# Performance work log

Hardware: AMD Instinct MI355X
Metric: run time of the kernel (lower is better)

Reference implementation:

```python
import jax, jax.numpy as jnp
import numpy as np

T, S, F, A = 256, 256, 1024, 256


def setup_inputs() -> dict:
    key = jax.random.key(0)
    ks = jax.random.split(key, 7)
    scale = 0.02
    return {
        "batch_data": jax.random.normal(ks[0], (T * S, F), dtype=jnp.float32),
        "a_w": jax.random.normal(ks[1], (F, A), dtype=jnp.float32) * scale,
        "a_b": jax.random.normal(ks[2], (A,), dtype=jnp.float32) * scale,
        "b_w": jax.random.normal(ks[3], (F, A), dtype=jnp.float32) * scale,
        "b_b": jax.random.normal(ks[4], (A,), dtype=jnp.float32) * scale,
        "g_w": jax.random.normal(ks[5], (F, F), dtype=jnp.float32) * scale,
        "g_b": jax.random.normal(ks[6], (F,), dtype=jnp.float32) * scale,
        "s": S,
        "t": T,
    }


def reference(batch_data, a_w, a_b, b_w, b_b, g_w, g_b, s, t):
    # Linear projections then reshape to (t, s, dim)
    theta = (batch_data @ a_w + a_b).reshape(t, s, -1)   # (t, s, A)
    phi = (batch_data @ b_w + b_b).reshape(t, s, -1)     # (t, s, A)
    feats = (batch_data @ g_w + g_b).reshape(t, s, -1)   # (t, s, F)
    # Per-t bilinear attention: theta @ phi^T, no softmax
    attn = jnp.einsum("tsa,tra->tsr", theta, phi)        # (t, s, s)
    results = jnp.einsum("tsr,trf->tsf", attn, feats)    # (t, s, F)
    return results / (s + t)
```

## Files before the change

### kernel.cpp

```cpp
#include <hip/hip_runtime.h>
#include <stdint.h>

#define TT 256
#define SS 256
#define FF 1024
#define AA 256

typedef __attribute__((ext_vector_type(8))) short short8;
typedef __attribute__((ext_vector_type(4))) float floatx4;

__device__ __forceinline__ unsigned short f2bf(float f) {
  unsigned int u = __float_as_uint(f);
  u += 0x7FFFu + ((u >> 16) & 1u);
  return (unsigned short)(u >> 16);
}

__device__ __forceinline__ void gl_lds16(const unsigned short* g, unsigned short* l) {
  __builtin_amdgcn_global_load_lds(
      (__attribute__((address_space(1))) void*)(g),
      (__attribute__((address_space(3))) void*)(l), 16, 0, 0);
}

__global__ void k_transpose_cvt(const float* __restrict__ W,
                                unsigned short* __restrict__ WT,
                                int K, int N) {
  __shared__ float tile[32][33];
  const int bk = blockIdx.x * 32, bn = blockIdx.y * 32;
  const int tx = threadIdx.x, ty = threadIdx.y;
  for (int i = ty; i < 32; i += 8)
    tile[i][tx] = W[(size_t)(bk + i) * N + bn + tx];
  __syncthreads();
  for (int i = ty; i < 32; i += 8)
    WT[(size_t)(bn + i) * K + bk + tx] = f2bf(tile[tx][i]);
}

__global__ __launch_bounds__(256) void k_cvt(const float* __restrict__ in,
                                             unsigned short* __restrict__ out,
                                             unsigned int n8) {
  unsigned int i = blockIdx.x * 256u + threadIdx.x;
  const unsigned int stride = gridDim.x * 256u;
  for (; i < n8; i += stride) {
    const size_t base = (size_t)i * 8;
    const floatx4 v0 = *(const floatx4*)(in + base);
    const floatx4 v1 = *(const floatx4*)(in + base + 4);
    ushort4 h0, h1;
    h0.x = f2bf(v0.x); h0.y = f2bf(v0.y); h0.z = f2bf(v0.z); h0.w = f2bf(v0.w);
    h1.x = f2bf(v1.x); h1.y = f2bf(v1.y); h1.z = f2bf(v1.z); h1.w = f2bf(v1.w);
    *(ushort4*)(out + base) = h0;
    *(ushort4*)(out + base + 4) = h1;
  }
}

__device__ __forceinline__ void stage_half(const unsigned short* G,
                                           unsigned short* L, int tid) {
  const int wave = tid >> 6, lane = tid & 63;
#pragma unroll
  for (int c = 0; c < 2; ++c) {
    const int chunk = c * 8 + wave;
    const int r = chunk * 8 + (lane >> 3);
    const int k8 = (lane & 7) ^ (lane >> 3);
    gl_lds16(G + (size_t)r * FF + k8 * 8, L + chunk * 512);
  }
}

__device__ __forceinline__ short8 ldsfrag(const unsigned short* h, int row,
                                          int col) {
  return *(const short8*)&h[row * 64 + (col ^ ((row & 7) << 3))];
}

__global__ __launch_bounds__(512, 2) void k_proj3(
    const unsigned short* __restrict__ batchH,
    const unsigned short* __restrict__ aT,
    const unsigned short* __restrict__ bT,
    const unsigned short* __restrict__ gT,
    const float* __restrict__ a_b, const float* __restrict__ b_b,
    const float* __restrict__ g_b,
    unsigned short* __restrict__ theta,
    unsigned short* __restrict__ phi,
    unsigned short* __restrict__ featsT,
    int mbase) {
  __shared__ unsigned short lds[65536];
  unsigned short* As = lds;
  unsigned short* Bs = lds + 32768;

  const int nwg = gridDim.x;
  const int hb = blockIdx.x;
  const int logical = (hb & 7) * (nwg >> 3) + (hb >> 3);
  const int nt = logical % 6;
  const int mtile = logical / 6;
  const int m0l = mtile * 256;
  const int m0 = mbase + m0l;

  const unsigned short* Wt; const float* bias; int nb0, mode;
  if (nt == 0)      { Wt = aT; bias = a_b; nb0 = 0;              mode = 0; }
  else if (nt == 1) { Wt = bT; bias = b_b; nb0 = 0;              mode = 1; }
  else              { Wt = gT; bias = g_b; nb0 = (nt - 2) * 256; mode = 2; }

  const int tid = threadIdx.x;
  const int wave = tid >> 6, lane = tid & 63;
  const int wm = wave >> 2, wn = wave & 3;
  const int lr = lane & 15, lq = lane >> 4;
  const int brow = (wn & 1) * 64;

  const unsigned short* Ap = batchH + (size_t)m0l * FF;
  const unsigned short* Bp = Wt + (size_t)nb0 * FF;

  floatx4 acc[8][4];
#pragma unroll
  for (int i = 0; i < 8; i++)
#pragma unroll
    for (int j = 0; j < 4; j++) acc[i][j] = (floatx4)0.0f;

  stage_half(Bp,                Bs + 0 * 8192, tid);
  stage_half(Bp + 128 * FF,     Bs + 1 * 8192, tid);
  stage_half(Ap,                As + 0 * 8192, tid);
  stage_half(Ap + 128 * FF,     As + 1 * 8192, tid);
  stage_half(Bp + 64,           Bs + 2 * 8192, tid);
  stage_half(Bp + 128 * FF + 64, Bs + 3 * 8192, tid);

  short8 af[4][2], bf[4][2];
  const int NKT = FF / 64;

#pragma unroll 1
  for (int kt = 0; kt < NKT; ++kt) {
    const unsigned short* Ah = As + ((kt & 1) * 2 + wm) * 8192;
    const unsigned short* Bh = Bs + ((kt & 1) * 2 + (wn >> 1)) * 8192;
    const int nbuf = 1 - (kt & 1);

    if (kt + 1 < NKT)
      stage_half(Ap + (size_t)(kt + 1) * 64, As + (nbuf * 2 + 0) * 8192, tid);
    if (kt + 1 < NKT) asm volatile("s_waitcnt vmcnt(6)" ::: "memory");
    else              asm volatile("s_waitcnt vmcnt(0)" ::: "memory");
    asm volatile("s_barrier" ::: "memory");
#pragma unroll
    for (int i = 0; i < 4; ++i)
#pragma unroll
      for (int ks = 0; ks < 2; ++ks)
        af[i][ks] = ldsfrag(Ah, i * 16 + lr, ks * 32 + lq * 8);
#pragma unroll
    for (int j = 0; j < 2; ++j)
#pragma unroll
      for (int ks = 0; ks < 2; ++ks)
        bf[j][ks] = ldsfrag(Bh, brow + j * 16 + lr, ks * 32 + lq * 8);
    __builtin_amdgcn_s_setprio(1);
#pragma unroll
    for (int i = 0; i < 4; ++i)
#pragma unroll
      for (int j = 0; j < 2; ++j)
#pragma unroll
        for (int ks = 0; ks < 2; ++ks)
          acc[i][j] = __builtin_amdgcn_mfma_f32_16x16x32_bf16(
              af[i][ks], bf[j][ks], acc[i][j], 0, 0, 0);
    __builtin_amdgcn_s_setprio(0);
    asm volatile("s_barrier" ::: "memory");

    if (kt + 1 < NKT)
      stage_half(Ap + 128 * FF + (size_t)(kt + 1) * 64,
                 As + (nbuf * 2 + 1) * 8192, tid);
#pragma unroll
    for (int j = 0; j < 2; ++j)
#pragma unroll
      for (int ks = 0; ks < 2; ++ks)
        bf[2 + j][ks] = ldsfrag(Bh, brow + (2 + j) * 16 + lr, ks * 32 + lq * 8);
    __builtin_amdgcn_s_setprio(1);
#pragma unroll
    for (int i = 0; i < 4; ++i)
#pragma unroll
      for (int j = 0; j < 2; ++j)
#pragma unroll
        for (int ks = 0; ks < 2; ++ks)
          acc[i][2 + j] = __builtin_amdgcn_mfma_f32_16x16x32_bf16(
              af[i][ks], bf[2 + j][ks], acc[i][2 + j], 0, 0, 0);
    __builtin_amdgcn_s_setprio(0);
    asm volatile("s_barrier" ::: "memory");

    if (kt + 2 < NKT)
      stage_half(Bp + (size_t)(kt + 2) * 64, Bs + ((kt & 1) * 2 + 0) * 8192,
                 tid);
#pragma unroll
    for (int i = 0; i < 4; ++i)
#pragma unroll
      for (int ks = 0; ks < 2; ++ks)
        af[i][ks] = ldsfrag(Ah, 64 + i * 16 + lr, ks * 32 + lq * 8);
    __builtin_amdgcn_s_setprio(1);
#pragma unroll
    for (int i = 0; i < 4; ++i)
#pragma unroll
      for (int j = 0; j < 2; ++j)
#pragma unroll
        for (int ks = 0; ks < 2; ++ks)
          acc[4 + i][j] = __builtin_amdgcn_mfma_f32_16x16x32_bf16(
              af[i][ks], bf[j][ks], acc[4 + i][j], 0, 0, 0);
    __builtin_amdgcn_s_setprio(0);
    asm volatile("s_barrier" ::: "memory");

    if (kt + 2 < NKT)
      stage_half(Bp + 128 * FF + (size_t)(kt + 2) * 64,
                 Bs + ((kt & 1) * 2 + 1) * 8192, tid);
    __builtin_amdgcn_s_setprio(1);
#pragma unroll
    for (int i = 0; i < 4; ++i)
#pragma unroll
      for (int j = 0; j < 2; ++j)
#pragma unroll
        for (int ks = 0; ks < 2; ++ks)
          acc[4 + i][2 + j] = __builtin_amdgcn_mfma_f32_16x16x32_bf16(
              af[i][ks], bf[2 + j][ks], acc[4 + i][2 + j], 0, 0, 0);
    __builtin_amdgcn_s_setprio(0);
    asm volatile("s_barrier" ::: "memory");
  }

#pragma unroll
  for (int fi = 0; fi < 8; ++fi) {
    const int srow = wm * 128 + fi * 16 + lq * 4;
#pragma unroll
    for (int j = 0; j < 4; ++j) {
      const int col = wn * 64 + j * 16 + lr;
      const float bv = bias[nb0 + col];
      if (mode == 2) {
        const int t = m0 >> 8;
        ushort4 h;
        h.x = f2bf(acc[fi][j][0] + bv);
        h.y = f2bf(acc[fi][j][1] + bv);
        h.z = f2bf(acc[fi][j][2] + bv);
        h.w = f2bf(acc[fi][j][3] + bv);
        *(ushort4*)&featsT[((size_t)t * FF + nb0 + col) * SS + srow] = h;
      } else {
        unsigned short* outp = (mode == 0) ? theta : phi;
#pragma unroll
        for (int rr = 0; rr < 4; ++rr)
          outp[(size_t)(m0 + srow + rr) * AA + col] = f2bf(acc[fi][j][rr] + bv);
      }
    }
  }
}

template <bool OUTF32>
__global__ __launch_bounds__(256) void k_gemm_bt(
    const unsigned short* __restrict__ A, const unsigned short* __restrict__ B,
    void* __restrict__ C, int N, int K, long sA, long sB, long sC,
    float scale) {
  __shared__ unsigned short As[128 * 32];
  __shared__ unsigned short Bs[128 * 32];

  const unsigned gx = gridDim.x, gy = gridDim.y;
  unsigned h = (blockIdx.z * gy + blockIdx.y) * gx + blockIdx.x;
  const unsigned nwg = gx * gy * gridDim.z;
  unsigned l = (nwg & 7) ? h : (h & 7) * (nwg >> 3) + (h >> 3);
  const unsigned bx = l % gx; l /= gx;
  const unsigned by = l % gy; const unsigned bz = l / gy;

  const unsigned short* Ab = A + (size_t)bz * sA;
  const unsigned short* Bb = B + (size_t)bz * sB;
  const int n0 = bx * 128, m0 = by * 128;
  const int tid = threadIdx.x, lane = tid & 63, wave = tid >> 6;
  const int wm = wave >> 1, wn = wave & 1, lr = lane & 15, lq = lane >> 4;

  floatx4 acc[4][4];
#pragma unroll
  for (int i = 0; i < 4; i++)
#pragma unroll
    for (int j = 0; j < 4; j++) acc[i][j] = (floatx4)0.0f;

  for (int k0 = 0; k0 < K; k0 += 32) {
    __syncthreads();
    int sl = tid;
    gl_lds16(Ab + (size_t)(m0 + (sl >> 2)) * K + k0 + (sl & 3) * 8,
             &As[wave * 512]);
    gl_lds16(Bb + (size_t)(n0 + (sl >> 2)) * K + k0 + (sl & 3) * 8,
             &Bs[wave * 512]);
    sl = tid + 256;
    gl_lds16(Ab + (size_t)(m0 + (sl >> 2)) * K + k0 + (sl & 3) * 8,
             &As[2048 + wave * 512]);
    gl_lds16(Bb + (size_t)(n0 + (sl >> 2)) * K + k0 + (sl & 3) * 8,
             &Bs[2048 + wave * 512]);
    __syncthreads();

    short8 af[4], bfr[4];
#pragma unroll
    for (int i = 0; i < 4; i++)
      af[i] = *(const short8*)&As[(wm * 64 + i * 16 + lr) * 32 + lq * 8];
#pragma unroll
    for (int j = 0; j < 4; j++)
      bfr[j] = *(const short8*)&Bs[(wn * 64 + j * 16 + lr) * 32 + lq * 8];
#pragma unroll
    for (int i = 0; i < 4; i++)
#pragma unroll
      for (int j = 0; j < 4; j++)
        acc[i][j] = __builtin_amdgcn_mfma_f32_16x16x32_bf16(af[i], bfr[j],
                                                            acc[i][j], 0, 0, 0);
  }

#pragma unroll
  for (int i = 0; i < 4; i++) {
    const int row0 = wm * 64 + i * 16 + lq * 4;
#pragma unroll
    for (int j = 0; j < 4; j++) {
      const int col = wn * 64 + j * 16 + lr;
#pragma unroll
      for (int rr = 0; rr < 4; rr++) {
        const float v = acc[i][j][rr] * scale;
        if (OUTF32) {
          float* Cb = (float*)C + (size_t)bz * sC;
          Cb[(size_t)(m0 + row0 + rr) * N + n0 + col] = v;
        } else {
          unsigned short* Cb = (unsigned short*)C + (size_t)bz * sC;
          Cb[(size_t)(m0 + row0 + rr) * N + n0 + col] = f2bf(v);
        }
      }
    }
  }
}

extern "C" void kernel_launch(void* const* d_in, const int* in_sizes, int n_in,
                              void* d_out, int out_size, void* d_ws,
                              size_t ws_size, hipStream_t stream) {
  const float* batch = (const float*)d_in[0];
  const float* a_w   = (const float*)d_in[1];
  const float* a_b   = (const float*)d_in[2];
  const float* b_w   = (const float*)d_in[3];
  const float* b_b   = (const float*)d_in[4];
  const float* g_w   = (const float*)d_in[5];
  const float* g_b   = (const float*)d_in[6];
  float* out = (float*)d_out;

  unsigned short* ws     = (unsigned short*)d_ws;
  unsigned short* aT     = ws;
  unsigned short* bT     = aT + (size_t)AA * FF;
  unsigned short* gT     = bT + (size_t)AA * FF;
  unsigned short* theta  = gT + (size_t)FF * FF;
  unsigned short* phi    = theta + (size_t)TT * SS * AA;
  unsigned short* featsT = phi + (size_t)TT * SS * AA;
  unsigned short* attn   = featsT + (size_t)TT * FF * SS;

  dim3 tb(32, 8);
  k_transpose_cvt<<<dim3(32, 8),  tb, 0, stream>>>(a_w, aT, FF, AA);
  k_transpose_cvt<<<dim3(32, 8),  tb, 0, stream>>>(b_w, bT, FF, AA);
  k_transpose_cvt<<<dim3(32, 32), tb, 0, stream>>>(g_w, gT, FF, FF);

  const size_t base_bytes  = 238026752ull;
  const size_t batch_bytes = (size_t)TT * SS * FF * 2;
  if (ws_size >= base_bytes + batch_bytes) {
    unsigned short* batchH = attn + (size_t)TT * SS * SS;
    k_cvt<<<2048, 256, 0, stream>>>(batch, batchH,
                                    (unsigned int)((size_t)TT * SS * FF / 8));
    k_proj3<<<6 * 256, 512, 0, stream>>>(batchH, aT, bT, gT, a_b, b_b, g_b,
                                         theta, phi, featsT, 0);
  } else {
    unsigned short* batchH = attn;
    const int CHUNK_ROWS = 16384;
    for (int c = 0; c < 4; c++) {
      const float* src = batch + (size_t)c * CHUNK_ROWS * FF;
      k_cvt<<<2048, 256, 0, stream>>>(
          src, batchH, (unsigned int)((size_t)CHUNK_ROWS * FF / 8));
      k_proj3<<<6 * 64, 512, 0, stream>>>(batchH, aT, bT, gT, a_b, b_b, g_b,
                                          theta, phi, featsT, c * CHUNK_ROWS);
    }
  }

  k_gemm_bt<false><<<dim3(2, 2, TT), 256, 0, stream>>>(
      theta, phi, attn, SS, AA, (long)SS * AA, (long)SS * AA, (long)SS * SS,
      1.0f);

  k_gemm_bt<true><<<dim3(8, 2, TT), 256, 0, stream>>>(
      attn, featsT, out, FF, SS, (long)SS * SS, (long)FF * SS, (long)SS * FF,
      1.0f / 512.0f);
}
```

Before: 439.5 us.

## Replace batched 128x128 attention GEMMs with shared pipelined 256x256 tile kernel

Factors the projection kernel's double-buffered 256x256 MFMA k-loop into macros with a configurable leading dimension. The two per-t batched GEMMs (theta·phiᵀ and attn·feats) now use this deeper-pipelined 512-thread 256x256 tile kernel instead of the simple 128x128 kernel that synchronised every 32-wide k-step. The aim is more data reuse and overlap of loads with compute. In exchange the grid is far smaller (256 and 1024 workgroups), and the projection k-loop now holds a separate af1 fragment set, which uses more registers.

```diff
diff --git a/kernel.cpp b/kernel.cpp
--- a/kernel.cpp
+++ b/kernel.cpp
@@ -51,7 +51,7 @@
   }
 }
 
-__device__ __forceinline__ void stage_half(const unsigned short* G,
+__device__ __forceinline__ void stage_half(const unsigned short* G, int ld,
                                            unsigned short* L, int tid) {
   const int wave = tid >> 6, lane = tid & 63;
 #pragma unroll
@@ -59,7 +59,7 @@
     const int chunk = c * 8 + wave;
     const int r = chunk * 8 + (lane >> 3);
     const int k8 = (lane & 7) ^ (lane >> 3);
-    gl_lds16(G + (size_t)r * FF + k8 * 8, L + chunk * 512);
+    gl_lds16(G + (size_t)r * ld + k8 * 8, L + chunk * 512);
   }
 }
 
@@ -67,6 +67,79 @@
                                           int col) {
   return *(const short8*)&h[row * 64 + (col ^ ((row & 7) << 3))];
 }
+
+#define KLOOP_256(Ap, ldA, Bp, ldB, NKT)                                       \
+  for (int kt = 0; kt < (NKT); ++kt) {                                         \
+    const unsigned short* Ah = As + ((kt & 1) * 2 + wm) * 8192;                \
+    const unsigned short* Bh = Bs + ((kt & 1) * 2 + (wn >> 1)) * 8192;         \
+    const int nbuf = 1 - (kt & 1);                                             \
+    if (kt + 1 < (NKT)) {                                                      \
+      stage_half((Ap) + (size_t)(kt + 1) * 64, (ldA),                          \
+                 As + (nbuf * 2 + 0) * 8192, tid);                             \
+      asm volatile("s_waitcnt vmcnt(6)" ::: "memory");                         \
+    } else {                                                                   \
+      asm volatile("s_waitcnt vmcnt(0)" ::: "memory");                         \
+    }                                                                          \
+    asm volatile("s_barrier" ::: "memory");                                    \
+    _Pragma("unroll") for (int i = 0; i < 4; ++i)                              \
+        _Pragma("unroll") for (int ks = 0; ks < 2; ++ks)                       \
+            af[i][ks] = ldsfrag(Ah, i * 16 + lr, ks * 32 + lq * 8);            \
+    _Pragma("unroll") for (int j = 0; j < 4; ++j)                              \
+        _Pragma("unroll") for (int ks = 0; ks < 2; ++ks)                       \
+            bf[j][ks] = ldsfrag(Bh, brow + j * 16 + lr, ks * 32 + lq * 8);     \
+    __builtin_amdgcn_s_setprio(1);                                             \
+    _Pragma("unroll") for (int i = 0; i < 4; ++i)                              \
+        _Pragma("unroll") for (int j = 0; j < 2; ++j)                          \
+            _Pragma("unroll") for (int ks = 0; ks < 2; ++ks)                   \
+                acc[i][j] = __builtin_amdgcn_mfma_f32_16x16x32_bf16(           \
+                    af[i][ks], bf[j][ks], acc[i][j], 0, 0, 0);                 \
+    __builtin_amdgcn_s_setprio(0);                                             \
+    asm volatile("s_barrier" ::: "memory");                                    \
+    if (kt + 1 < (NKT))                                                        \
+      stage_half((Ap) + 128 * (ldA) + (size_t)(kt + 1) * 64, (ldA),            \
+                 As + (nbuf * 2 + 1) * 8192, tid);                             \
+    _Pragma("unroll") for (int i = 0; i < 4; ++i)                              \
+        _Pragma("unroll") for (int ks = 0; ks < 2; ++ks)                       \
+            af1[i][ks] = ldsfrag(Ah, 64 + i * 16 + lr, ks * 32 + lq * 8);      \
+    __builtin_amdgcn_s_setprio(1);                                             \
+    _Pragma("unroll") for (int i = 0; i < 4; ++i)                              \
+        _Pragma("unroll") for (int j = 0; j < 2; ++j)                          \
+            _Pragma("unroll") for (int ks = 0; ks < 2; ++ks)                   \
+                acc[i][2 + j] = __builtin_amdgcn_mfma_f32_16x16x32_bf16(       \
+                    af[i][ks], bf[2 + j][ks], acc[i][2 + j], 0, 0, 0);         \
+    __builtin_amdgcn_s_setprio(0);                                             \
+    asm volatile("s_barrier" ::: "memory");                                    \
+    if (kt + 2 < (NKT))                                                        \
+      stage_half((Bp) + (size_t)(kt + 2) * 64, (ldB),                          \
+                 Bs + ((kt & 1) * 2 + 0) * 8192, tid);                         \
+    __builtin_amdgcn_s_setprio(1);                                             \
+    _Pragma("unroll") for (int i = 0; i < 4; ++i)                              \
+        _Pragma("unroll") for (int j = 0; j < 2; ++j)                          \
+            _Pragma("unroll") for (int ks = 0; ks < 2; ++ks)                   \
+                acc[4 + i][j] = __builtin_amdgcn_mfma_f32_16x16x32_bf16(       \
+                    af1[i][ks], bf[j][ks], acc[4 + i][j], 0, 0, 0);            \
+    __builtin_amdgcn_s_setprio(0);                                             \
+    asm volatile("s_barrier" ::: "memory");                                    \
+    if (kt + 2 < (NKT))                                                        \
+      stage_half((Bp) + 128 * (ldB) + (size_t)(kt + 2) * 64, (ldB),            \
+                 Bs + ((kt & 1) * 2 + 1) * 8192, tid);                         \
+    __builtin_amdgcn_s_setprio(1);                                             \
+    _Pragma("unroll") for (int i = 0; i < 4; ++i)                              \
+        _Pragma("unroll") for (int j = 0; j < 2; ++j)                          \
+            _Pragma("unroll") for (int ks = 0; ks < 2; ++ks)                   \
+                acc[4 + i][2 + j] = __builtin_amdgcn_mfma_f32_16x16x32_bf16(   \
+                    af1[i][ks], bf[2 + j][ks], acc[4 + i][2 + j], 0, 0, 0);    \
+    __builtin_amdgcn_s_setprio(0);                                             \
+    asm volatile("s_barrier" ::: "memory");                                    \
+  }
+
+#define PROLOGUE_256(Ap, ldA, Bp, ldB)                                         \
+  stage_half((Bp), (ldB), Bs + 0 * 8192, tid);                                 \
+  stage_half((Bp) + 128 * (ldB), (ldB), Bs + 1 * 8192, tid);                   \
+  stage_half((Ap), (ldA), As + 0 * 8192, tid);                                 \
+  stage_half((Ap) + 128 * (ldA), (ldA), As + 1 * 8192, tid);                   \
+  stage_half((Bp) + 64, (ldB), Bs + 2 * 8192, tid);                            \
+  stage_half((Bp) + 128 * (ldB) + 64, (ldB), Bs + 3 * 8192, tid);
 
 __global__ __launch_bounds__(512, 2) void k_proj3(
     const unsigned short* __restrict__ batchH,
@@ -111,104 +184,11 @@
 #pragma unroll
     for (int j = 0; j < 4; j++) acc[i][j] = (floatx4)0.0f;
 
-  stage_half(Bp,                Bs + 0 * 8192, tid);
-  stage_half(Bp + 128 * FF,     Bs + 1 * 8192, tid);
-  stage_half(Ap,                As + 0 * 8192, tid);
-  stage_half(Ap + 128 * FF,     As + 1 * 8192, tid);
-  stage_half(Bp + 64,           Bs + 2 * 8192, tid);
-  stage_half(Bp + 128 * FF + 64, Bs + 3 * 8192, tid);
-
-  short8 af[4][2], bf[4][2];
-  const int NKT = FF / 64;
-
+  short8 af[4][2], af1[4][2], bf[4][2];
+
+  PROLOGUE_256(Ap, FF, Bp, FF)
 #pragma unroll 1
-  for (int kt = 0; kt < NKT; ++kt) {
-    const unsigned short* Ah = As + ((kt & 1) * 2 + wm) * 8192;
-    const unsigned short* Bh = Bs + ((kt & 1) * 2 + (wn >> 1)) * 8192;
-    const int nbuf = 1 - (kt & 1);
-
-    if (kt + 1 < NKT)
-      stage_half(Ap + (size_t)(kt + 1) * 64, As + (nbuf * 2 + 0) * 8192, tid);
-    if (kt + 1 < NKT) asm volatile("s_waitcnt vmcnt(6)" ::: "memory");
-    else              asm volatile("s_waitcnt vmcnt(0)" ::: "memory");
-    asm volatile("s_barrier" ::: "memory");
-#pragma unroll
-    for (int i = 0; i < 4; ++i)
-#pragma unroll
-      for (int ks = 0; ks < 2; ++ks)
-        af[i][ks] = ldsfrag(Ah, i * 16 + lr, ks * 32 + lq * 8);
-#pragma unroll
-    for (int j = 0; j < 2; ++j)
-#pragma unroll
-      for (int ks = 0; ks < 2; ++ks)
-        bf[j][ks] = ldsfrag(Bh, brow + j * 16 + lr, ks * 32 + lq * 8);
-    __builtin_amdgcn_s_setprio(1);
-#pragma unroll
-    for (int i = 0; i < 4; ++i)
-#pragma unroll
-      for (int j = 0; j < 2; ++j)
-#pragma unroll
-        for (int ks = 0; ks < 2; ++ks)
-          acc[i][j] = __builtin_amdgcn_mfma_f32_16x16x32_bf16(
-              af[i][ks], bf[j][ks], acc[i][j], 0, 0, 0);
-    __builtin_amdgcn_s_setprio(0);
-    asm volatile("s_barrier" ::: "memory");
-
-    if (kt + 1 < NKT)
-      stage_half(Ap + 128 * FF + (size_t)(kt + 1) * 64,
-                 As + (nbuf * 2 + 1) * 8192, tid);
-#pragma unroll
-    for (int j = 0; j < 2; ++j)
-#pragma unroll
-      for (int ks = 0; ks < 2; ++ks)
-        bf[2 + j][ks] = ldsfrag(Bh, brow + (2 + j) * 16 + lr, ks * 32 + lq * 8);
-    __builtin_amdgcn_s_setprio(1);
-#pragma unroll
-    for (int i = 0; i < 4; ++i)
-#pragma unroll
-      for (int j = 0; j < 2; ++j)
-#pragma unroll
-        for (int ks = 0; ks < 2; ++ks)
-          acc[i][2 + j] = __builtin_amdgcn_mfma_f32_16x16x32_bf16(
-              af[i][ks], bf[2 + j][ks], acc[i][2 + j], 0, 0, 0);
-    __builtin_amdgcn_s_setprio(0);
-    asm volatile("s_barrier" ::: "memory");
-
-    if (kt + 2 < NKT)
-      stage_half(Bp + (size_t)(kt + 2) * 64, Bs + ((kt & 1) * 2 + 0) * 8192,
-                 tid);
-#pragma unroll
-    for (int i = 0; i < 4; ++i)
-#pragma unroll
-      for (int ks = 0; ks < 2; ++ks)
-        af[i][ks] = ldsfrag(Ah, 64 + i * 16 + lr, ks * 32 + lq * 8);
-    __builtin_amdgcn_s_setprio(1);
-#pragma unroll
-    for (int i = 0; i < 4; ++i)
-#pragma unroll
-      for (int j = 0; j < 2; ++j)
-#pragma unroll
-        for (int ks = 0; ks < 2; ++ks)
-          acc[4 + i][j] = __builtin_amdgcn_mfma_f32_16x16x32_bf16(
-              af[i][ks], bf[j][ks], acc[4 + i][j], 0, 0, 0);
-    __builtin_amdgcn_s_setprio(0);
-    asm volatile("s_barrier" ::: "memory");
-
-    if (kt + 2 < NKT)
-      stage_half(Bp + 128 * FF + (size_t)(kt + 2) * 64,
-                 Bs + ((kt & 1) * 2 + 1) * 8192, tid);
-    __builtin_amdgcn_s_setprio(1);
-#pragma unroll
-    for (int i = 0; i < 4; ++i)
-#pragma unroll
-      for (int j = 0; j < 2; ++j)
-#pragma unroll
-        for (int ks = 0; ks < 2; ++ks)
-          acc[4 + i][2 + j] = __builtin_amdgcn_mfma_f32_16x16x32_bf16(
-              af[i][ks], bf[2 + j][ks], acc[4 + i][2 + j], 0, 0, 0);
-    __builtin_amdgcn_s_setprio(0);
-    asm volatile("s_barrier" ::: "memory");
-  }
+  KLOOP_256(Ap, FF, Bp, FF, FF / 64)
 
 #pragma unroll
   for (int fi = 0; fi < 8; ++fi) {
@@ -236,76 +216,58 @@
 }
 
 template <bool OUTF32>
-__global__ __launch_bounds__(256) void k_gemm_bt(
+__global__ __launch_bounds__(512, 2) void k_bt256(
     const unsigned short* __restrict__ A, const unsigned short* __restrict__ B,
-    void* __restrict__ C, int N, int K, long sA, long sB, long sC,
-    float scale) {
-  __shared__ unsigned short As[128 * 32];
-  __shared__ unsigned short Bs[128 * 32];
-
-  const unsigned gx = gridDim.x, gy = gridDim.y;
-  unsigned h = (blockIdx.z * gy + blockIdx.y) * gx + blockIdx.x;
-  const unsigned nwg = gx * gy * gridDim.z;
-  unsigned l = (nwg & 7) ? h : (h & 7) * (nwg >> 3) + (h >> 3);
-  const unsigned bx = l % gx; l /= gx;
-  const unsigned by = l % gy; const unsigned bz = l / gy;
-
-  const unsigned short* Ab = A + (size_t)bz * sA;
-  const unsigned short* Bb = B + (size_t)bz * sB;
-  const int n0 = bx * 128, m0 = by * 128;
-  const int tid = threadIdx.x, lane = tid & 63, wave = tid >> 6;
-  const int wm = wave >> 1, wn = wave & 1, lr = lane & 15, lq = lane >> 4;
-
-  floatx4 acc[4][4];
-#pragma unroll
-  for (int i = 0; i < 4; i++)
+    void* __restrict__ C, int ldA, int ldB, int K,
+    long sA, long sB, long sC, int ntiles, float scale) {
+  __shared__ unsigned short lds[65536];
+  unsigned short* As = lds;
+  unsigned short* Bs = lds + 32768;
+
+  const int nwg = gridDim.x;
+  const int hb = blockIdx.x;
+  const int logical = (nwg & 7) ? hb : (hb & 7) * (nwg >> 3) + (hb >> 3);
+  const int bz = logical / ntiles;
+  const int n0 = (logical % ntiles) * 256;
+
+  const int tid = threadIdx.x;
+  const int wave = tid >> 6, lane = tid & 63;
+  const int wm = wave >> 2, wn = wave & 3;
+  const int lr = lane & 15, lq = lane >> 4;
+  const int brow = (wn & 1) * 64;
+
+  const unsigned short* Ap = A + (size_t)bz * sA;
+  const unsigned short* Bp = B + (size_t)bz * sB + (size_t)n0 * ldB;
+
+  floatx4 acc[8][4];
+#pragma unroll
+  for (int i = 0; i < 8; i++)
 #pragma unroll
     for (int j = 0; j < 4; j++) acc[i][j] = (floatx4)0.0f;
 
-  for (int k0 = 0; k0 < K; k0 += 32) {
-    __syncthreads();
-    int sl = tid;
-    gl_lds16(Ab + (size_t)(m0 + (sl >> 2)) * K + k0 + (sl & 3) * 8,
-             &As[wave * 512]);
-    gl_lds16(Bb + (size_t)(n0 + (sl >> 2)) * K + k0 + (sl & 3) * 8,
-             &Bs[wave * 512]);
-    sl = tid + 256;
-    gl_lds16(Ab + (size_t)(m0 + (sl >> 2)) * K + k0 + (sl & 3) * 8,
-             &As[2048 + wave * 512]);
-    gl_lds16(Bb + (size_t)(n0 + (sl >> 2)) * K + k0 + (sl & 3) * 8,
-             &Bs[2048 + wave * 512]);
-    __syncthreads();
-
-    short8 af[4], bfr[4];
-#pragma unroll
-    for (int i = 0; i < 4; i++)
-      af[i] = *(const short8*)&As[(wm * 64 + i * 16 + lr) * 32 + lq * 8];
-#pragma unroll
-    for (int j = 0; j < 4; j++)
-      bfr[j] = *(const short8*)&Bs[(wn * 64 + j * 16 + lr) * 32 + lq * 8];
-#pragma unroll
-    for (int i = 0; i < 4; i++)
-#pragma unroll
-      for (int j = 0; j < 4; j++)
-        acc[i][j] = __builtin_amdgcn_mfma_f32_16x16x32_bf16(af[i], bfr[j],
-                                                            acc[i][j], 0, 0, 0);
-  }
-
-#pragma unroll
-  for (int i = 0; i < 4; i++) {
-    const int row0 = wm * 64 + i * 16 + lq * 4;
-#pragma unroll
-    for (int j = 0; j < 4; j++) {
-      const int col = wn * 64 + j * 16 + lr;
-#pragma unroll
-      for (int rr = 0; rr < 4; rr++) {
-        const float v = acc[i][j][rr] * scale;
+  short8 af[4][2], af1[4][2], bf[4][2];
+  const int NKT = K / 64;
+
+  PROLOGUE_256(Ap, ldA, Bp, ldB)
+#pragma unroll 1
+  KLOOP_256(Ap, ldA, Bp, ldB, NKT)
+
+  const int ldC = ntiles * 256;
+#pragma unroll
+  for (int fi = 0; fi < 8; ++fi) {
+    const int srow = wm * 128 + fi * 16 + lq * 4;
+#pragma unroll
+    for (int j = 0; j < 4; ++j) {
+      const int col = n0 + wn * 64 + j * 16 + lr;
+#pragma unroll
+      for (int rr = 0; rr < 4; ++rr) {
+        const float v = acc[fi][j][rr] * scale;
         if (OUTF32) {
           float* Cb = (float*)C + (size_t)bz * sC;
-          Cb[(size_t)(m0 + row0 + rr) * N + n0 + col] = v;
+          Cb[(size_t)(srow + rr) * ldC + col] = v;
         } else {
           unsigned short* Cb = (unsigned short*)C + (size_t)bz * sC;
-          Cb[(size_t)(m0 + row0 + rr) * N + n0 + col] = f2bf(v);
+          Cb[(size_t)(srow + rr) * ldC + col] = f2bf(v);
         }
       }
     }
@@ -358,11 +320,11 @@
     }
   }
 
-  k_gemm_bt<false><<<dim3(2, 2, TT), 256, 0, stream>>>(
-      theta, phi, attn, SS, AA, (long)SS * AA, (long)SS * AA, (long)SS * SS,
-      1.0f);
-
-  k_gemm_bt<true><<<dim3(8, 2, TT), 256, 0, stream>>>(
-      attn, featsT, out, FF, SS, (long)SS * SS, (long)FF * SS, (long)SS * FF,
-      1.0f / 512.0f);
-}
+  k_bt256<false><<<TT, 512, 0, stream>>>(
+      theta, phi, attn, AA, AA, AA,
+      (long)SS * AA, (long)SS * AA, (long)SS * SS, 1, 1.0f);
+
+  k_bt256<true><<<4 * TT, 512, 0, stream>>>(
+      attn, featsT, out, SS, SS, SS,
+      (long)SS * SS, (long)FF * SS, (long)SS * FF, 4, 1.0f / 512.0f);
+}
```

New measurement: 434.6 us. No clear change (-1.1%).
